# Kernel tuning notes

Measured on AMD Instinct MI355X. Metric: run time of the kernel, lower is better.

## Reference

```python
import jax, jax.numpy as jnp
import numpy as np
from math import pi, sqrt, factorial

NUM_SPHERICAL = 7
NUM_RADIAL = 6
CUTOFF = 5.0


def _sph_jn_np(x, n):
    # spherical Bessel j_n(x) in float64 numpy via upward recurrence
    x = np.asarray(x, dtype=np.float64)
    jm = np.sin(x) / x
    if n == 0:
        return jm
    jc = np.sin(x) / x**2 - np.cos(x) / x
    for l in range(2, n + 1):
        jm, jc = jc, (2 * l - 1) / x * jc - jm
    return jc


def _jn_zeros(n, k):
    # first k positive zeros of j_l for l = 0..n-1 (zeros of j_l interleave those of j_{l-1})
    nz = k + n
    z = np.zeros((n, nz))
    z[0] = np.arange(1, nz + 1) * np.pi
    for l in range(1, n):
        for j in range(nz - l):
            a, b = z[l - 1, j], z[l - 1, j + 1]
            fa = _sph_jn_np(a, l)
            for _ in range(100):
                m = 0.5 * (a + b)
                fm = _sph_jn_np(m, l)
                if fa * fm <= 0:
                    b = m
                else:
                    a, fa = m, fm
            z[l, j] = 0.5 * (a + b)
    return z[:, :k]


_ZEROS_NP = _jn_zeros(NUM_SPHERICAL, NUM_RADIAL)  # (n, k)
_NORM_NP = np.array([[(0.5 * _sph_jn_np(_ZEROS_NP[l, j], l + 1) ** 2) ** -0.5
                      for j in range(NUM_RADIAL)] for l in range(NUM_SPHERICAL)])
BESSEL_ZEROS = jnp.asarray(_ZEROS_NP, dtype=jnp.float32)  # z_{l,j}
BESSEL_NORM = jnp.asarray(_NORM_NP, dtype=jnp.float32)    # sqrt(2)/|j_{l+1}(z_{l,j})|


def _rbf(dist):
    # normalized spherical Bessel basis: rbf[:, l*k + j] = norm[l,j] * j_l(z_{l,j} * dist/cutoff)
    d = dist / CUTOFF
    u = d[:, None, None] * BESSEL_ZEROS[None]  # (E, n, k)
    cols = []
    for l in range(NUM_SPHERICAL):
        x = u[:, l, :]
        jm = jnp.sin(x) / x  # j_0
        if l == 0:
            jc = jm
        else:
            jc = jnp.sin(x) / (x * x) - jnp.cos(x) / x  # j_1
        for ll in range(2, l + 1):
            jm, jc = jc, (2 * ll - 1) / x * jc - jm
        cols.append(BESSEL_NORM[l] * jc)
    return jnp.concatenate(cols, axis=1)  # (E, n*k)


def _cbf(angle, phi):
    # real spherical harmonics Y_{l,m}(angle, phi), flat order m = -l..l per l
    n = NUM_SPHERICAL
    z = jnp.cos(angle)
    s = jnp.sin(angle)
    P = {(0, 0): jnp.ones_like(z)}
    for m in range(1, n):
        P[(m, m)] = (1 - 2 * m) * s * P[(m - 1, m - 1)]  # Condon-Shortley phase included
    for m in range(0, n - 1):
        P[(m + 1, m)] = (2 * m + 1) * z * P[(m, m)]
    for m in range(n):
        for l in range(m + 2, n):
            P[(l, m)] = ((2 * l - 1) * z * P[(l - 1, m)] - (l + m - 1) * P[(l - 2, m)]) / (l - m)

    def pref(l, m):
        return sqrt((2 * l + 1) * factorial(l - m) / (4.0 * pi * factorial(l + m)))

    cols = [jnp.full_like(angle, 0.5 / sqrt(pi))]  # Y_00 constant
    for l in range(1, n):
        for m in range(-l, l + 1):
            am = abs(m)
            if m < 0:
                cols.append(sqrt(2.0) * pref(l, am) * jnp.sin(am * phi) * P[(l, am)])
            elif m == 0:
                cols.append(pref(l, 0) * P[(l, 0)])
            else:
                cols.append(sqrt(2.0) * pref(l, am) * jnp.cos(am * phi) * P[(l, am)])
    return jnp.stack(cols, axis=1)  # (T, n*n)


def setup_inputs() -> dict:
    key = jax.random.key(0)
    kd, ka, kp, ki = jax.random.split(key, 4)
    E, T = 150000, 500000
    dist = jax.random.uniform(kd, (E,), minval=0.5, maxval=5.0, dtype=jnp.float32)
    angle = jax.random.uniform(ka, (T,), minval=0.0, maxval=float(np.pi), dtype=jnp.float32)
    phi = jax.random.uniform(kp, (T,), minval=-float(np.pi), maxval=float(np.pi), dtype=jnp.float32)
    idx_kj = jax.random.randint(ki, (T,), 0, E)
    return {"dist": dist, "angle": angle, "phi": phi, "idx_kj": idx_kj}


def reference(dist, angle, phi, idx_kj):
    n, k = NUM_SPHERICAL, NUM_RADIAL
    rbf = _rbf(dist)          # (E, n*k)
    cbf = _cbf(angle, phi)    # (T, n*n)
    out = (rbf[idx_kj].reshape(-1, 1, n, k) * cbf.reshape(-1, n, n, 1)).reshape(-1, n * n * k)
    return out
```

## Files before the change

### kernel.cpp

```cpp
#include <hip/hip_runtime.h>
#include <math.h>

#ifndef M_PI
#define M_PI 3.14159265358979323846
#endif

#define NS 7
#define NK 6
#define GT 64
#define BT 256
#define NC (NS*NS)
#define NR (NS*NK)
#define NF2 147

typedef float f32x2 __attribute__((ext_vector_type(2)));
typedef float f32x4 __attribute__((ext_vector_type(4)));


__device__ void jl_pair_f(float x, int l, float& jl, float& jm1) {
  float s, c;
  __sincosf(x, &s, &c);
  float invx = 1.0f / x;
  float j0 = s * invx, jm = c * invx;
  if (l == 0) { jl = j0; jm1 = jm; return; }
  float j1 = (s * invx - c) * invx;
  for (int ll = 2; ll <= l; ++ll) {
    float t = (2.0f * ll - 1.0f) * invx * j1 - j0;
    j0 = j1; j1 = t;
  }
  jl = j1; jm1 = j0;
}

__global__ void setup_kernel(float* tab) {
  int id = threadIdx.x;
  if (id < NS * NK) {
    int l = id / NK, j = id % NK;
    float nu = l + 0.5f, mu = 4.0f * nu * nu;
    float b  = ((float)(j + 1) + 0.5f * nu - 0.25f) * (float)M_PI;
    float b8 = 8.0f * b;
    float x = b - (mu - 1.0f) / b8
                - 4.0f * (mu - 1.0f) * (7.0f * mu - 31.0f) / (3.0f * b8 * b8 * b8)
                - 32.0f * (mu - 1.0f) * (83.0f * mu * mu - 982.0f * mu + 3779.0f) /
                  (15.0f * b8 * b8 * b8 * b8 * b8);
    float jl, jm1;
    for (int it = 0; it < 5; ++it) {
      jl_pair_f(x, l, jl, jm1);
      float dj = jm1 - (l + 1.0f) / x * jl;
      x -= jl / dj;
    }
    tab[id] = x;
    jl_pair_f(x, l, jl, jm1);
    float jp1 = (2.0f * l + 1.0f) / x * jl - jm1;
    tab[NS * NK + id] = sqrtf(2.0f) / fabsf(jp1);
  }
  if (id < NC) {
    double v;
    if (id == 0) {
      v = 0.5 / sqrt(M_PI);
    } else {
      int l = 1;
      while ((l + 1) * (l + 1) <= id) ++l;
      int m  = id - l * l - l;
      int am = m < 0 ? -m : m;
      double fr = 1.0;
      for (int i2 = l - am + 1; i2 <= l + am; ++i2) fr *= (double)i2;
      double pref = sqrt((2.0 * l + 1.0) / (4.0 * M_PI * fr));
      v = (m != 0) ? sqrt(2.0) * pref : pref;
    }
    tab[2 * NS * NK + id] = (float)v;
  }
}

__global__ __launch_bounds__(BT, 4) void torsion_kernel(
    const float* __restrict__ dist, const float* __restrict__ angle,
    const float* __restrict__ phi, const int* __restrict__ idx_kj,
    const float* __restrict__ tab, float* __restrict__ out, int T) {
  __shared__ float s_cbf[GT][NC];
  __shared__ __align__(8) float s_rbf[GT][NR];
  __shared__ float s_d[GT];
  __shared__ float s_tab[133];
  __shared__ unsigned s_map2[NF2];

  const int tid = threadIdx.x;
  const int t0  = blockIdx.x * GT;
  const int nt  = min(GT, T - t0);

  float a = 0.0f, ph = 0.0f;
  if (tid < GT) {
    int t = t0 + tid;
    float dd = 1.0f;
    if (t < T) {
      dd = dist[idx_kj[t]] * 0.2f;
      a  = angle[t];
      ph = phi[t];
    }
    s_d[tid] = dd;
  }
  if (tid < 133) s_tab[tid] = tab[tid];
  if (tid < NF2) {
    auto mk = [](int cc) {
      int ii = (cc * 3121) >> 16;
      int rem2 = cc - 21 * ii;
      int jj = (rem2 * 86) >> 8;
      return (unsigned)((ii * NS + jj) | (rem2 << 8));
    };
    int cc1 = tid + 1; if (cc1 == NF2) cc1 = 0;
    s_map2[tid] = mk(tid) | (mk(cc1) << 16);
  }
  __syncthreads();

  if (tid < GT) {
    if (t0 + tid < T) {
      float z = cosf(a), s = sinf(a);
      float sp, cp;
      sincosf(ph, &sp, &cp);
      float cmv[NS], smv[NS];
      cmv[0] = 1.0f; smv[0] = 0.0f;
      cmv[1] = cp;   smv[1] = sp;
#pragma unroll
      for (int m = 2; m < NS; ++m) {
        cmv[m] = 2.0f * cp * cmv[m - 1] - cmv[m - 2];
        smv[m] = 2.0f * cp * smv[m - 1] - smv[m - 2];
      }
      const float* coef = s_tab + 2 * NR;
      float* crow = s_cbf[tid];
      float pmm = 1.0f;
#pragma unroll
      for (int m = 0; m < NS; ++m) {
        float pl1 = pmm, pl2 = 0.0f;
#pragma unroll
        for (int l = m; l < NS; ++l) {
          float plm;
          if (l == m)          plm = pmm;
          else if (l == m + 1) plm = (float)(2 * m + 1) * z * pmm;
          else                 plm = ((float)(2 * l - 1) * z * pl1 -
                                      (float)(l + m - 1) * pl2) *
                                     (float)(1.0 / (double)(l - m));
          int cpn = l * l + l + m;
          if (m == 0) {
            crow[cpn] = coef[cpn] * plm;
          } else {
            crow[cpn] = coef[cpn] * cmv[m] * plm;
            crow[l * l + l - m] = coef[l * l + l - m] * smv[m] * plm;
          }
          pl2 = pl1; pl1 = plm;
        }
        pmm = (float)(-1 - 2 * m) * s * pmm;
      }
    }
  } else {
    int j  = tid - 64;
    int t  = j / NR;
    int cc = j - NR * t;
    int i2 = j;
    float* rlin = &s_rbf[0][0];
#pragma unroll 2
    for (int it = 0; it < 14; ++it) {
      int l = (cc * 43) >> 8;
      float x = s_d[t] * s_tab[cc];
      float sx, cx;
      sincosf(x, &sx, &cx);
      float invx = 1.0f / x;
      float jm = sx * invx;
      float jc;
      if (l == 0) jc = jm;
      else {
        jc = (sx * invx - cx) * invx;
#pragma unroll
        for (int ll = 2; ll <= 6; ++ll) {
          if (ll <= l) {
            float tt = (float)(2 * ll - 1) * invx * jc - jm;
            jm = jc; jc = tt;
          }
        }
      }
      rlin[i2] = s_tab[NR + cc] * jc;
      i2 += 192;
      cc += 24; t += 4;
      if (cc >= NR) { cc -= NR; ++t; }
    }
  }
  __syncthreads();

  const f32x2* r2 = (const f32x2*)&s_rbf[0][0];

  if (nt == GT) {
    f32x4* o4 = (f32x4*)out + (size_t)blockIdx.x * 4704 + tid;

    int k = tid, p = 0;
    if (k >= NF2) { k -= NF2; p = 1; }

    unsigned m[18];
    {
      int cc = k << 1; if (cc >= NF2) cc -= NF2;
#pragma unroll
      for (int it = 0; it < 18; ++it) {
        m[it] = s_map2[cc];
        cc += 71; if (cc >= NF2) cc -= NF2;
      }
    }

    float cva[3], cvb[3];
    f32x2 rva[3], rvb[3];
    int ki = k, pi = p;

    auto ISSUE = [&](int slot, int it) {
      int t2 = pi << 1;
      int ta = t2 + (ki >= 74 ? 1 : 0);
      int tb = t2 + (ki >= 73 ? 1 : 0);
      unsigned mp = m[it];
      unsigned i0 = mp & 0xffu,          r0 = (mp >> 8) & 0xffu;
      unsigned i1 = (mp >> 16) & 0xffu,  r1 = mp >> 24;
      cva[slot] = s_cbf[ta][i0];
      rva[slot] = r2[ta * 21 + r0];
      cvb[slot] = s_cbf[tb][i1];
      rvb[slot] = r2[tb * 21 + r1];
      ki += 109; ++pi;
      if (ki >= NF2) { ki -= NF2; ++pi; }
    };

    ISSUE(0, 0);
    ISSUE(1, 1);
#pragma unroll
    for (int it = 0; it < 18; ++it) {
      if (it + 2 < 18) ISSUE((it + 2) % 3, it + 2);
      int sl = it % 3;
      f32x4 ov = {cva[sl] * rva[sl].x, cva[sl] * rva[sl].y,
                  cvb[sl] * rvb[sl].x, cvb[sl] * rvb[sl].y};
      __builtin_nontemporal_store(ov, o4 + it * 256);
    }

    if (tid < 96) {
      int cc = ki << 1; if (cc >= NF2) cc -= NF2;
      unsigned mp = s_map2[cc];
      int t2 = pi << 1;
      int ta = t2 + (ki >= 74 ? 1 : 0);
      int tb = t2 + (ki >= 73 ? 1 : 0);
      unsigned i0 = mp & 0xffu,          r0 = (mp >> 8) & 0xffu;
      unsigned i1 = (mp >> 16) & 0xffu,  r1 = mp >> 24;
      float cv0 = s_cbf[ta][i0];
      f32x2 rv0 = r2[ta * 21 + r0];
      float cv1 = s_cbf[tb][i1];
      f32x2 rv1 = r2[tb * 21 + r1];
      f32x4 ov = {cv0 * rv0.x, cv0 * rv0.y, cv1 * rv1.x, cv1 * rv1.y};
      __builtin_nontemporal_store(ov, o4 + 18 * 256);
    }
  } else {
    f32x2* o2 = (f32x2*)out + (size_t)t0 * NF2;
    int tot = nt * NF2;
    for (int i = tid; i < tot; i += BT) {
      int t  = i / NF2;
      int c2 = i - NF2 * t;
      unsigned mp = s_map2[c2] & 0xffffu;
      float cv = s_cbf[t][mp & 0xffu];
      f32x2 rv = r2[t * 21 + (mp >> 8)];
      f32x2 ov = cv * rv;
      __builtin_nontemporal_store(ov, o2 + i);
    }
  }
}

extern "C" void kernel_launch(void* const* d_in, const int* in_sizes, int n_in,
                              void* d_out, int out_size, void* d_ws, size_t ws_size,
                              hipStream_t stream) {
  const float* dist  = (const float*)d_in[0];
  const float* angle = (const float*)d_in[1];
  const float* phi   = (const float*)d_in[2];
  const int*   idx   = (const int*)d_in[3];
  float* out = (float*)d_out;
  float* tab = (float*)d_ws;
  int T = in_sizes[1];

  hipLaunchKernelGGL(setup_kernel, dim3(1), dim3(64), 0, stream, tab);
  int nb = (T + GT - 1) / GT;
  hipLaunchKernelGGL(torsion_kernel, dim3(nb), dim3(BT), 0, stream,
                     dist, angle, phi, idx, tab, out, T);
}
```

Baseline: 127.2 us.

## Process four tiles per block with double-buffered shared memory

```diff
diff --git a/kernel.cpp b/kernel.cpp
--- a/kernel.cpp
+++ b/kernel.cpp
@@ -9,6 +9,7 @@
 #define NK 6
 #define GT 64
 #define BT 256
+#define TPB 4
 #define NC (NS*NS)
 #define NR (NS*NK)
 #define NF2 147
@@ -71,31 +72,21 @@
   }
 }
 
-__global__ __launch_bounds__(BT, 4) void torsion_kernel(
+__global__ __launch_bounds__(BT, 3) void torsion_kernel(
     const float* __restrict__ dist, const float* __restrict__ angle,
     const float* __restrict__ phi, const int* __restrict__ idx_kj,
     const float* __restrict__ tab, float* __restrict__ out, int T) {
-  __shared__ float s_cbf[GT][NC];
-  __shared__ __align__(8) float s_rbf[GT][NR];
-  __shared__ float s_d[GT];
+  __shared__ float s_cbf[2][GT][NC];
+  __shared__ __align__(8) float s_rbf[2][GT][NR];
+  __shared__ float s_d[2][GT];
   __shared__ float s_tab[133];
   __shared__ unsigned s_map2[NF2];
 
-  const int tid = threadIdx.x;
-  const int t0  = blockIdx.x * GT;
-  const int nt  = min(GT, T - t0);
-
-  float a = 0.0f, ph = 0.0f;
-  if (tid < GT) {
-    int t = t0 + tid;
-    float dd = 1.0f;
-    if (t < T) {
-      dd = dist[idx_kj[t]] * 0.2f;
-      a  = angle[t];
-      ph = phi[t];
-    }
-    s_d[tid] = dd;
-  }
+  const int tid   = threadIdx.x;
+  const int ntt   = (T + GT - 1) / GT;
+  const int tile0 = blockIdx.x * TPB;
+  if (tile0 >= ntt) return;
+
   if (tid < 133) s_tab[tid] = tab[tid];
   if (tid < NF2) {
     auto mk = [](int cc) {
@@ -107,156 +98,193 @@
     int cc1 = tid + 1; if (cc1 == NF2) cc1 = 0;
     s_map2[tid] = mk(tid) | (mk(cc1) << 16);
   }
+
+  float a0 = 0.0f, p0 = 0.0f;
+  if (tid < GT) {
+    int t = tile0 * GT + tid;
+    float dd = 1.0f;
+    if (t < T) {
+      a0 = angle[t]; p0 = phi[t];
+      dd = dist[idx_kj[t]] * 0.2f;
+    }
+    s_d[0][tid] = dd;
+  }
   __syncthreads();
 
-  if (tid < GT) {
-    if (t0 + tid < T) {
-      float z = cosf(a), s = sinf(a);
-      float sp, cp;
-      sincosf(ph, &sp, &cp);
-      float cmv[NS], smv[NS];
-      cmv[0] = 1.0f; smv[0] = 0.0f;
-      cmv[1] = cp;   smv[1] = sp;
-#pragma unroll
-      for (int m = 2; m < NS; ++m) {
-        cmv[m] = 2.0f * cp * cmv[m - 1] - cmv[m - 2];
-        smv[m] = 2.0f * cp * smv[m - 1] - smv[m - 2];
-      }
-      const float* coef = s_tab + 2 * NR;
-      float* crow = s_cbf[tid];
-      float pmm = 1.0f;
-#pragma unroll
-      for (int m = 0; m < NS; ++m) {
-        float pl1 = pmm, pl2 = 0.0f;
-#pragma unroll
-        for (int l = m; l < NS; ++l) {
-          float plm;
-          if (l == m)          plm = pmm;
-          else if (l == m + 1) plm = (float)(2 * m + 1) * z * pmm;
-          else                 plm = ((float)(2 * l - 1) * z * pl1 -
-                                      (float)(l + m - 1) * pl2) *
-                                     (float)(1.0 / (double)(l - m));
-          int cpn = l * l + l + m;
-          if (m == 0) {
-            crow[cpn] = coef[cpn] * plm;
-          } else {
-            crow[cpn] = coef[cpn] * cmv[m] * plm;
-            crow[l * l + l - m] = coef[l * l + l - m] * smv[m] * plm;
+  unsigned m[18];
+  int k_st = tid, p_st = 0;
+  if (k_st >= NF2) { k_st -= NF2; p_st = 1; }
+  {
+    int cc = k_st << 1; if (cc >= NF2) cc -= NF2;
+#pragma unroll
+    for (int it = 0; it < 18; ++it) {
+      m[it] = s_map2[cc];
+      cc += 71; if (cc >= NF2) cc -= NF2;
+    }
+  }
+
+  auto COMPUTE = [&](int b, int ti, float a, float ph) {
+    if (tid < GT) {
+      if (ti * GT + tid < T) {
+        float z = cosf(a), s = sinf(a);
+        float sp, cp;
+        sincosf(ph, &sp, &cp);
+        float cmv[NS], smv[NS];
+        cmv[0] = 1.0f; smv[0] = 0.0f;
+        cmv[1] = cp;   smv[1] = sp;
+#pragma unroll
+        for (int mm = 2; mm < NS; ++mm) {
+          cmv[mm] = 2.0f * cp * cmv[mm - 1] - cmv[mm - 2];
+          smv[mm] = 2.0f * cp * smv[mm - 1] - smv[mm - 2];
+        }
+        const float* coef = s_tab + 2 * NR;
+        float* crow = s_cbf[b][tid];
+        float pmm = 1.0f;
+#pragma unroll
+        for (int mm = 0; mm < NS; ++mm) {
+          float pl1 = pmm, pl2 = 0.0f;
+#pragma unroll
+          for (int l = mm; l < NS; ++l) {
+            float plm;
+            if (l == mm)          plm = pmm;
+            else if (l == mm + 1) plm = (float)(2 * mm + 1) * z * pmm;
+            else                  plm = ((float)(2 * l - 1) * z * pl1 -
+                                         (float)(l + mm - 1) * pl2) *
+                                        (float)(1.0 / (double)(l - mm));
+            int cpn = l * l + l + mm;
+            if (mm == 0) {
+              crow[cpn] = coef[cpn] * plm;
+            } else {
+              crow[cpn] = coef[cpn] * cmv[mm] * plm;
+              crow[l * l + l - mm] = coef[l * l + l - mm] * smv[mm] * plm;
+            }
+            pl2 = pl1; pl1 = plm;
           }
-          pl2 = pl1; pl1 = plm;
+          pmm = (float)(-1 - 2 * mm) * s * pmm;
         }
-        pmm = (float)(-1 - 2 * m) * s * pmm;
-      }
-    }
-  } else {
-    int j  = tid - 64;
-    int t  = j / NR;
-    int cc = j - NR * t;
-    int i2 = j;
-    float* rlin = &s_rbf[0][0];
+      }
+    } else {
+      int j  = tid - 64;
+      int t  = j / NR;
+      int cc = j - NR * t;
+      int i2 = j;
+      float* rlin = &s_rbf[b][0][0];
+      const float* sd = s_d[b];
 #pragma unroll 2
-    for (int it = 0; it < 14; ++it) {
-      int l = (cc * 43) >> 8;
-      float x = s_d[t] * s_tab[cc];
-      float sx, cx;
-      sincosf(x, &sx, &cx);
-      float invx = 1.0f / x;
-      float jm = sx * invx;
-      float jc;
-      if (l == 0) jc = jm;
-      else {
-        jc = (sx * invx - cx) * invx;
-#pragma unroll
-        for (int ll = 2; ll <= 6; ++ll) {
-          if (ll <= l) {
-            float tt = (float)(2 * ll - 1) * invx * jc - jm;
-            jm = jc; jc = tt;
+      for (int it = 0; it < 14; ++it) {
+        int l = (cc * 43) >> 8;
+        float x = sd[t] * s_tab[cc];
+        float sx, cx;
+        sincosf(x, &sx, &cx);
+        float invx = 1.0f / x;
+        float jm = sx * invx;
+        float jc;
+        if (l == 0) jc = jm;
+        else {
+          jc = (sx * invx - cx) * invx;
+#pragma unroll
+          for (int ll = 2; ll <= 6; ++ll) {
+            if (ll <= l) {
+              float tt = (float)(2 * ll - 1) * invx * jc - jm;
+              jm = jc; jc = tt;
+            }
           }
         }
-      }
-      rlin[i2] = s_tab[NR + cc] * jc;
-      i2 += 192;
-      cc += 24; t += 4;
-      if (cc >= NR) { cc -= NR; ++t; }
-    }
-  }
-  __syncthreads();
-
-  const f32x2* r2 = (const f32x2*)&s_rbf[0][0];
-
-  if (nt == GT) {
-    f32x4* o4 = (f32x4*)out + (size_t)blockIdx.x * 4704 + tid;
-
-    int k = tid, p = 0;
-    if (k >= NF2) { k -= NF2; p = 1; }
-
-    unsigned m[18];
-    {
-      int cc = k << 1; if (cc >= NF2) cc -= NF2;
+        rlin[i2] = s_tab[NR + cc] * jc;
+        i2 += 192;
+        cc += 24; t += 4;
+        if (cc >= NR) { cc -= NR; ++t; }
+      }
+    }
+  };
+
+  COMPUTE(0, tile0, a0, p0);
+
+  for (int k2 = 0; k2 < TPB; ++k2) {
+    int ti = tile0 + k2;
+    if (ti >= ntt) break;
+    int cur = k2 & 1;
+    bool havenext = (k2 + 1 < TPB) && (ti + 1 < ntt);
+
+    float a1 = 0.0f, p1 = 0.0f, dd1 = 1.0f;
+    if (havenext && tid < GT) {
+      int t1 = (ti + 1) * GT + tid;
+      if (t1 < T) {
+        a1 = angle[t1]; p1 = phi[t1];
+        dd1 = dist[idx_kj[t1]] * 0.2f;
+      }
+    }
+    __syncthreads();
+
+    int nt = min(GT, T - ti * GT);
+    const f32x2* r2 = (const f32x2*)&s_rbf[cur][0][0];
+    const float (*cb)[NC] = s_cbf[cur];
+
+    if (nt == GT) {
+      f32x4* o4 = (f32x4*)out + (size_t)ti * 4704 + tid;
+
+      float cva[3], cvb[3];
+      f32x2 rva[3], rvb[3];
+      int ki = k_st, pi = p_st;
+
+      auto ISSUE = [&](int slot, int it) {
+        int t2 = pi << 1;
+        int ta = t2 + (ki >= 74 ? 1 : 0);
+        int tb = t2 + (ki >= 73 ? 1 : 0);
+        unsigned mp = m[it];
+        unsigned i0 = mp & 0xffu,          r0 = (mp >> 8) & 0xffu;
+        unsigned i1 = (mp >> 16) & 0xffu,  r1 = mp >> 24;
+        cva[slot] = cb[ta][i0];
+        rva[slot] = r2[ta * 21 + r0];
+        cvb[slot] = cb[tb][i1];
+        rvb[slot] = r2[tb * 21 + r1];
+        ki += 109; ++pi;
+        if (ki >= NF2) { ki -= NF2; ++pi; }
+      };
+
+      ISSUE(0, 0);
+      ISSUE(1, 1);
 #pragma unroll
       for (int it = 0; it < 18; ++it) {
-        m[it] = s_map2[cc];
-        cc += 71; if (cc >= NF2) cc -= NF2;
-      }
-    }
-
-    float cva[3], cvb[3];
-    f32x2 rva[3], rvb[3];
-    int ki = k, pi = p;
-
-    auto ISSUE = [&](int slot, int it) {
-      int t2 = pi << 1;
-      int ta = t2 + (ki >= 74 ? 1 : 0);
-      int tb = t2 + (ki >= 73 ? 1 : 0);
-      unsigned mp = m[it];
-      unsigned i0 = mp & 0xffu,          r0 = (mp >> 8) & 0xffu;
-      unsigned i1 = (mp >> 16) & 0xffu,  r1 = mp >> 24;
-      cva[slot] = s_cbf[ta][i0];
-      rva[slot] = r2[ta * 21 + r0];
-      cvb[slot] = s_cbf[tb][i1];
-      rvb[slot] = r2[tb * 21 + r1];
-      ki += 109; ++pi;
-      if (ki >= NF2) { ki -= NF2; ++pi; }
-    };
-
-    ISSUE(0, 0);
-    ISSUE(1, 1);
-#pragma unroll
-    for (int it = 0; it < 18; ++it) {
-      if (it + 2 < 18) ISSUE((it + 2) % 3, it + 2);
-      int sl = it % 3;
-      f32x4 ov = {cva[sl] * rva[sl].x, cva[sl] * rva[sl].y,
-                  cvb[sl] * rvb[sl].x, cvb[sl] * rvb[sl].y};
-      __builtin_nontemporal_store(ov, o4 + it * 256);
-    }
-
-    if (tid < 96) {
-      int cc = ki << 1; if (cc >= NF2) cc -= NF2;
-      unsigned mp = s_map2[cc];
-      int t2 = pi << 1;
-      int ta = t2 + (ki >= 74 ? 1 : 0);
-      int tb = t2 + (ki >= 73 ? 1 : 0);
-      unsigned i0 = mp & 0xffu,          r0 = (mp >> 8) & 0xffu;
-      unsigned i1 = (mp >> 16) & 0xffu,  r1 = mp >> 24;
-      float cv0 = s_cbf[ta][i0];
-      f32x2 rv0 = r2[ta * 21 + r0];
-      float cv1 = s_cbf[tb][i1];
-      f32x2 rv1 = r2[tb * 21 + r1];
-      f32x4 ov = {cv0 * rv0.x, cv0 * rv0.y, cv1 * rv1.x, cv1 * rv1.y};
-      __builtin_nontemporal_store(ov, o4 + 18 * 256);
-    }
-  } else {
-    f32x2* o2 = (f32x2*)out + (size_t)t0 * NF2;
-    int tot = nt * NF2;
-    for (int i = tid; i < tot; i += BT) {
-      int t  = i / NF2;
-      int c2 = i - NF2 * t;
-      unsigned mp = s_map2[c2] & 0xffffu;
-      float cv = s_cbf[t][mp & 0xffu];
-      f32x2 rv = r2[t * 21 + (mp >> 8)];
-      f32x2 ov = cv * rv;
-      __builtin_nontemporal_store(ov, o2 + i);
-    }
+        if (it + 2 < 18) ISSUE((it + 2) % 3, it + 2);
+        int sl = it % 3;
+        f32x4 ov = {cva[sl] * rva[sl].x, cva[sl] * rva[sl].y,
+                    cvb[sl] * rvb[sl].x, cvb[sl] * rvb[sl].y};
+        __builtin_nontemporal_store(ov, o4 + it * 256);
+      }
+
+      if (tid < 96) {
+        int cc = ki << 1; if (cc >= NF2) cc -= NF2;
+        unsigned mp = s_map2[cc];
+        int t2 = pi << 1;
+        int ta = t2 + (ki >= 74 ? 1 : 0);
+        int tb = t2 + (ki >= 73 ? 1 : 0);
+        unsigned i0 = mp & 0xffu,          r0 = (mp >> 8) & 0xffu;
+        unsigned i1 = (mp >> 16) & 0xffu,  r1 = mp >> 24;
+        float cv0 = cb[ta][i0];
+        f32x2 rv0 = r2[ta * 21 + r0];
+        float cv1 = cb[tb][i1];
+        f32x2 rv1 = r2[tb * 21 + r1];
+        f32x4 ov = {cv0 * rv0.x, cv0 * rv0.y, cv1 * rv1.x, cv1 * rv1.y};
+        __builtin_nontemporal_store(ov, o4 + 18 * 256);
+      }
+    } else {
+      f32x2* o2 = (f32x2*)out + (size_t)ti * GT * NF2;
+      int tot = nt * NF2;
+      for (int i = tid; i < tot; i += BT) {
+        int t  = i / NF2;
+        int c2 = i - NF2 * t;
+        unsigned mp = s_map2[c2] & 0xffffu;
+        float cv = cb[t][mp & 0xffu];
+        f32x2 rv = r2[t * 21 + (mp >> 8)];
+        f32x2 ov = cv * rv;
+        __builtin_nontemporal_store(ov, o2 + i);
+      }
+    }
+
+    if (havenext && tid < GT) s_d[(k2 + 1) & 1][tid] = dd1;
+    __syncthreads();
+    if (havenext) COMPUTE((k2 + 1) & 1, ti + 1, a1, p1);
   }
 }
 
@@ -272,7 +300,8 @@
   int T = in_sizes[1];
 
   hipLaunchKernelGGL(setup_kernel, dim3(1), dim3(64), 0, stream, tab);
-  int nb = (T + GT - 1) / GT;
+  int ntt = (T + GT - 1) / GT;
+  int nb  = (ntt + TPB - 1) / TPB;
   hipLaunchKernelGGL(torsion_kernel, dim3(nb), dim3(BT), 0, stream,
                      dist, angle, phi, idx, tab, out, T);
 }
```

Measured after the change: 155.3 us. 22.1% more time.
